# Kernel optimization log

Measured on AMD Instinct MI355X. Metric: run time of the kernel, lower is better.

The kernel has to match this reference:

```python
import jax, jax.numpy as jnp
import numpy as np

NEG_BIG = 10000000000.0  # matches tf source's -1e10 mask fill


def setup_inputs() -> dict:
    key = jax.random.key(0)
    k1, k2, k3 = jax.random.split(key, 3)
    B, H, T, D = 2, 12, 4096, 64
    return {
        "q": jax.random.normal(k1, (B, H, T, D), dtype=jnp.float32),
        "k": jax.random.normal(k2, (B, H, T, D), dtype=jnp.float32),
        "v": jax.random.normal(k3, (B, H, T, D), dtype=jnp.float32),
        "localAttention": 256,
    }


def _band_mask(nd, ns, local_attention, dtype):
    # 1's in the lower triangle counting from the lower-right corner,
    # optionally restricted to a local window of width `local_attention`.
    i = jnp.arange(nd)[:, None]
    j = jnp.arange(ns)[None, :]
    m = i >= j - ns + nd
    if local_attention > 0:
        m = m & (i < j - ns + nd + local_attention)
    return m.astype(dtype)


def reference(q, k, v, localAttention):
    # q,k,v: [B, H, T, D]
    dimv = v.shape[-1]
    w = jnp.einsum("bhqd,bhkd->bhqk", q, k) * (1.0 / np.sqrt(dimv))
    nd, ns = w.shape[2], w.shape[3]
    b = _band_mask(nd, ns, localAttention, w.dtype)[None, None]  # [1,1,nd,ns]
    w = w * b - jnp.asarray(NEG_BIG, w.dtype) * (1 - b)
    sm = jax.nn.softmax(w, axis=-1)
    out = jnp.einsum("bhqk,bhkd->bhqd", sm, v)       # [B,H,T,Dv]
    out = jnp.transpose(out, (0, 2, 1, 3))            # [B,T,H,Dv]
    B, T, H, Dv = out.shape
    return out.reshape(B, T, H * Dv)
```

## Files before the change

### kernel.cpp

```cpp
#include <hip/hip_runtime.h>

#define TT 4096
#define DD 64
#define HH 12
#define LAMAX 256
#define KT 64
#define VS 68

typedef __attribute__((ext_vector_type(8))) short s8v;
typedef __attribute__((ext_vector_type(4))) short s4v;
typedef __attribute__((ext_vector_type(2))) short s2v;
typedef __attribute__((ext_vector_type(4))) float f4v;

static __device__ __forceinline__ short f2bf(float f) {
  unsigned u = __builtin_bit_cast(unsigned, f);
  u += 0x7FFFu + ((u >> 16) & 1u);
  return (short)(u >> 16);
}

static __device__ __forceinline__ s8v pack8(float4 a, float4 b) {
  s8v r;
  r[0] = f2bf(a.x); r[1] = f2bf(a.y); r[2] = f2bf(a.z); r[3] = f2bf(a.w);
  r[4] = f2bf(b.x); r[5] = f2bf(b.y); r[6] = f2bf(b.z); r[7] = f2bf(b.w);
  return r;
}

static __device__ __forceinline__ s8v pack8s(float4 a, float4 b, float s) {
  s8v r;
  r[0] = f2bf(a.x * s); r[1] = f2bf(a.y * s); r[2] = f2bf(a.z * s); r[3] = f2bf(a.w * s);
  r[4] = f2bf(b.x * s); r[5] = f2bf(b.y * s); r[6] = f2bf(b.z * s); r[7] = f2bf(b.w * s);
  return r;
}

static __device__ __forceinline__ f4v MFMA16(s4v a, s4v b, f4v c) {
#if defined(__has_builtin) && __has_builtin(__builtin_amdgcn_mfma_f32_16x16x16bf16_1k)
  return __builtin_amdgcn_mfma_f32_16x16x16bf16_1k(a, b, c, 0, 0, 0);
#elif defined(__has_builtin) && __has_builtin(__builtin_amdgcn_mfma_f32_16x16x16_bf16)
  return __builtin_amdgcn_mfma_f32_16x16x16_bf16(a, b, c, 0, 0, 0);
#else
  asm("v_mfma_f32_16x16x16_bf16 %0, %1, %2, %0\n\ts_nop 7\n\ts_nop 7"
      : "+v"(c) : "v"(a), "v"(b));
  return c;
#endif
}

__global__ __launch_bounds__(256, 4)
void lma_attn_kernel(const float* __restrict__ Q, const float* __restrict__ K,
                     const float* __restrict__ V, const int* __restrict__ laPtr,
                     float* __restrict__ out)
{
  __shared__ short k_lds[2][64 * 64];
  __shared__ short vt_lds[2][64 * VS];

  const int tid  = threadIdx.x;
  const int lane = tid & 63;
  const int w    = tid >> 6;
  const int c    = lane & 15;
  const int g    = lane >> 4;

  const int bid = blockIdx.x;
  const int wg  = (bid & 7) * 192 + (bid >> 3);
  const int bh  = wg >> 6;
  const int q0  = (wg & 63) << 6;
  const int la  = laPtr[0];

  const size_t base = (size_t)bh * (TT * DD);
  const int rb    = q0 + w * 16;
  const int i_row = rb + c;

  const float SCL = 0.125f * 1.44269504f;
  s8v qf[2];
  {
    const float* qp = Q + base + (size_t)i_row * DD + 8 * g;
    qf[0] = pack8s(*(const float4*)qp,        *(const float4*)(qp + 4),  SCL);
    qf[1] = pack8s(*(const float4*)(qp + 32), *(const float4*)(qp + 36), SCL);
  }

  const int kj  = tid >> 2;
  const int kd0 = (tid & 3) << 4;
  const int vj0 = (tid & 31) << 1;
  const int vd0 = (tid >> 5) << 3;

  float4 kr0, kr1, kr2, kr3, vr0, vr1, vr2, vr3;
  auto stage_load = [&](int kj0) {
    const float* kp = K + base + (size_t)(kj0 + kj) * DD + kd0;
    kr0 = *(const float4*)kp;        kr1 = *(const float4*)(kp + 4);
    kr2 = *(const float4*)(kp + 8);  kr3 = *(const float4*)(kp + 12);
    const float* vp = V + base + (size_t)(kj0 + vj0) * DD + vd0;
    vr0 = *(const float4*)vp;        vr1 = *(const float4*)(vp + 4);
    vr2 = *(const float4*)(vp + DD); vr3 = *(const float4*)(vp + DD + 4);
  };
  auto stage_write = [&](int buf) {
    short* kb = (short*)k_lds[buf];
    const int sw = kj & 7, g8 = kd0 >> 3;
    *(s8v*)&kb[kj * 64 + ((g8    ) ^ sw) * 8] = pack8(kr0, kr1);
    *(s8v*)&kb[kj * 64 + ((g8 + 1) ^ sw) * 8] = pack8(kr2, kr3);
    short* vb = (short*)vt_lds[buf];
    const float a0[8] = {vr0.x, vr0.y, vr0.z, vr0.w, vr1.x, vr1.y, vr1.z, vr1.w};
    const float a1[8] = {vr2.x, vr2.y, vr2.z, vr2.w, vr3.x, vr3.y, vr3.z, vr3.w};
    #pragma unroll
    for (int e = 0; e < 8; ++e) {
      s2v pr; pr[0] = f2bf(a0[e]); pr[1] = f2bf(a1[e]);
      *(s2v*)&vb[(vd0 + e) * VS + vj0] = pr;
    }
  };

  f4v acc[4] = {};
  float m2   = -1e30f;
  float lsum = 0.f;

  const int t0 = (q0 >= LAMAX) ? 0 : ((LAMAX - q0) >> 6);

  stage_load(q0 - LAMAX + (t0 << 6));
  stage_write(t0 & 1);
  __syncthreads();

  for (int t = t0; t < 5; ++t) {
    const int kj0 = q0 - LAMAX + (t << 6);
    if (t < 4) stage_load(kj0 + KT);

    const short* kb = (const short*)k_lds[t & 1];
    const short* vb = (const short*)vt_lds[t & 1];

    if ((kj0 <= rb + 15) && (kj0 + KT >= rb - la + 2)) {
      f4v sa[4] = {};
      #pragma unroll
      for (int ch = 0; ch < 2; ++ch)
        #pragma unroll
        for (int ks = 0; ks < 4; ++ks) {
          s8v kf = *(const s8v*)&kb[(ks * 16 + c) * 64 + (((ch << 2) + g) ^ (c & 7)) * 8];
          sa[ks] = __builtin_amdgcn_mfma_f32_16x16x32_bf16(kf, qf[ch], sa[ks], 0, 0, 0);
        }

      const bool needC = (kj0 + 63 > rb);
      const bool needL = (kj0 < rb + 16 - la);
      const int jrel = kj0 - rb;
      const int jloR = i_row - la + 1;
      float p[4][4];
      #define MASKMAX(NC, NL)                                              \
        _Pragma("unroll")                                                  \
        for (int ks = 0; ks < 4; ++ks)                                     \
          _Pragma("unroll")                                                \
          for (int r = 0; r < 4; ++r) {                                    \
            float s = sa[ks][r];                                           \
            if (NC || NL) {                                                \
              const int jt = kj0 + ks * 16 + 4 * g + r;                    \
              bool ok = true;                                              \
              if (NC) ok = (jt <= i_row);                                  \
              if (NL) ok = ok && (jt >= jloR);                             \
              s = ok ? s : -1e30f;                                         \
            }                                                              \
            p[ks][r] = s;                                                  \
          }
      if (needC) { if (needL) { MASKMAX(true, true) } else { MASKMAX(true, false) } }
      else       { if (needL) { MASKMAX(false, true) } else { MASKMAX(false, false) } }
      #undef MASKMAX
      (void)jrel;

      float t0a = fmaxf(fmaxf(p[0][0], p[0][1]), fmaxf(p[0][2], p[0][3]));
      float t1a = fmaxf(fmaxf(p[1][0], p[1][1]), fmaxf(p[1][2], p[1][3]));
      float t2a = fmaxf(fmaxf(p[2][0], p[2][1]), fmaxf(p[2][2], p[2][3]));
      float t3a = fmaxf(fmaxf(p[3][0], p[3][1]), fmaxf(p[3][2], p[3][3]));
      float tmax = fmaxf(fmaxf(t0a, t1a), fmaxf(t2a, t3a));
      tmax = fmaxf(tmax, __shfl_xor(tmax, 16, 64));
      tmax = fmaxf(tmax, __shfl_xor(tmax, 32, 64));

      if (!__all(tmax <= m2 + 8.0f)) {
        const float mn = fmaxf(m2, tmax);
        const float corr = exp2f(m2 - mn);
        m2 = mn;
        lsum *= corr;
        #pragma unroll
        for (int dt = 0; dt < 4; ++dt) {
          acc[dt][0] *= corr; acc[dt][1] *= corr;
          acc[dt][2] *= corr; acc[dt][3] *= corr;
        }
      }

      s4v pb[4]; float e[4][4];
      #pragma unroll
      for (int ks = 0; ks < 4; ++ks)
        #pragma unroll
        for (int r = 0; r < 4; ++r) {
          e[ks][r] = exp2f(p[ks][r] - m2);
          pb[ks][r] = f2bf(e[ks][r]);
        }

      #pragma unroll
      for (int dt = 0; dt < 4; ++dt) {
        const int d = dt * 16 + c;
        #pragma unroll
        for (int sub = 0; sub < 4; ++sub) {
          s4v vf = *(const s4v*)&vb[d * VS + sub * 16 + g * 4];
          acc[dt] = MFMA16(vf, pb[sub], acc[dt]);
        }
      }

      float s0 = (e[0][0] + e[0][1]) + (e[0][2] + e[0][3]);
      float s1 = (e[1][0] + e[1][1]) + (e[1][2] + e[1][3]);
      float s2 = (e[2][0] + e[2][1]) + (e[2][2] + e[2][3]);
      float s3 = (e[3][0] + e[3][1]) + (e[3][2] + e[3][3]);
      float ps = (s0 + s1) + (s2 + s3);
      ps += __shfl_xor(ps, 16, 64);
      ps += __shfl_xor(ps, 32, 64);
      lsum += ps;
    }

    if (t < 4) stage_write((t + 1) & 1);
    __syncthreads();
  }

  const float inv = 1.f / lsum;
  float* op = out + ((size_t)(bh / HH) * TT + i_row) * (HH * DD) + (bh % HH) * DD + 4 * g;
  #pragma unroll
  for (int dt = 0; dt < 4; ++dt) {
    float4 o;
    o.x = acc[dt][0] * inv; o.y = acc[dt][1] * inv;
    o.z = acc[dt][2] * inv; o.w = acc[dt][3] * inv;
    *(float4*)(op + dt * 16) = o;
  }
}

extern "C" void kernel_launch(void* const* d_in, const int* in_sizes, int n_in,
                              void* d_out, int out_size, void* d_ws, size_t ws_size,
                              hipStream_t stream) {
  const float* q = (const float*)d_in[0];
  const float* k = (const float*)d_in[1];
  const float* v = (const float*)d_in[2];
  const int* la = (const int*)d_in[3];
  float* out = (float*)d_out;
  (void)in_sizes; (void)n_in; (void)out_size; (void)d_ws; (void)ws_size;

  dim3 grid(24 * 64);
  dim3 block(256);
  lma_attn_kernel<<<grid, block, 0, stream>>>(q, k, v, la, out);
}
```

Measured before the change: 143.2 us.

## Halve key tile to 32 rows, use packed bf16 conversion and raise occupancy

Shrinks the K/V tile from 64 to 32 keys and runs 10 iterations instead of 5, so blocks skip more of the band that lies outside the mask and use less LDS and fewer registers. Launch bounds rise to 6 waves per SIMD. Scalar bf16 rounding is replaced with packed float2-to-bf16 conversion and the hardware exp2 builtin. The XCD-aware block remap is removed. In exchange there are more barriers and more, smaller loads per output row.

```diff
diff --git a/kernel.cpp b/kernel.cpp
--- a/kernel.cpp
+++ b/kernel.cpp
@@ -1,42 +1,43 @@
 #include <hip/hip_runtime.h>
+#include <hip/hip_bf16.h>
 
 #define TT 4096
 #define DD 64
 #define HH 12
 #define LAMAX 256
-#define KT 64
-#define VS 68
+#define KT 32
+#define NT 10
+#define VS 36
 
 typedef __attribute__((ext_vector_type(8))) short s8v;
 typedef __attribute__((ext_vector_type(4))) short s4v;
 typedef __attribute__((ext_vector_type(2))) short s2v;
 typedef __attribute__((ext_vector_type(4))) float f4v;
 
-static __device__ __forceinline__ short f2bf(float f) {
-  unsigned u = __builtin_bit_cast(unsigned, f);
-  u += 0x7FFFu + ((u >> 16) & 1u);
-  return (short)(u >> 16);
+static __device__ __forceinline__ unsigned pk2(float a, float b) {
+  __hip_bfloat162 h = __float22bfloat162_rn(make_float2(a, b));
+  unsigned u;
+  __builtin_memcpy(&u, &h, sizeof(u));
+  return u;
 }
 
 static __device__ __forceinline__ s8v pack8(float4 a, float4 b) {
-  s8v r;
-  r[0] = f2bf(a.x); r[1] = f2bf(a.y); r[2] = f2bf(a.z); r[3] = f2bf(a.w);
-  r[4] = f2bf(b.x); r[5] = f2bf(b.y); r[6] = f2bf(b.z); r[7] = f2bf(b.w);
-  return r;
+  union { unsigned u[4]; s8v s; } r;
+  r.u[0] = pk2(a.x, a.y); r.u[1] = pk2(a.z, a.w);
+  r.u[2] = pk2(b.x, b.y); r.u[3] = pk2(b.z, b.w);
+  return r.s;
 }
 
 static __device__ __forceinline__ s8v pack8s(float4 a, float4 b, float s) {
-  s8v r;
-  r[0] = f2bf(a.x * s); r[1] = f2bf(a.y * s); r[2] = f2bf(a.z * s); r[3] = f2bf(a.w * s);
-  r[4] = f2bf(b.x * s); r[5] = f2bf(b.y * s); r[6] = f2bf(b.z * s); r[7] = f2bf(b.w * s);
-  return r;
+  union { unsigned u[4]; s8v r; } o;
+  o.u[0] = pk2(a.x * s, a.y * s); o.u[1] = pk2(a.z * s, a.w * s);
+  o.u[2] = pk2(b.x * s, b.y * s); o.u[3] = pk2(b.z * s, b.w * s);
+  return o.r;
 }
 
 static __device__ __forceinline__ f4v MFMA16(s4v a, s4v b, f4v c) {
 #if defined(__has_builtin) && __has_builtin(__builtin_amdgcn_mfma_f32_16x16x16bf16_1k)
   return __builtin_amdgcn_mfma_f32_16x16x16bf16_1k(a, b, c, 0, 0, 0);
-#elif defined(__has_builtin) && __has_builtin(__builtin_amdgcn_mfma_f32_16x16x16_bf16)
-  return __builtin_amdgcn_mfma_f32_16x16x16_bf16(a, b, c, 0, 0, 0);
 #else
   asm("v_mfma_f32_16x16x16_bf16 %0, %1, %2, %0\n\ts_nop 7\n\ts_nop 7"
       : "+v"(c) : "v"(a), "v"(b));
@@ -44,12 +45,12 @@
 #endif
 }
 
-__global__ __launch_bounds__(256, 4)
+__global__ __launch_bounds__(256, 6)
 void lma_attn_kernel(const float* __restrict__ Q, const float* __restrict__ K,
                      const float* __restrict__ V, const int* __restrict__ laPtr,
                      float* __restrict__ out)
 {
-  __shared__ short k_lds[2][64 * 64];
+  __shared__ short k_lds[2][KT * 64];
   __shared__ short vt_lds[2][64 * VS];
 
   const int tid  = threadIdx.x;
@@ -59,9 +60,8 @@
   const int g    = lane >> 4;
 
   const int bid = blockIdx.x;
-  const int wg  = (bid & 7) * 192 + (bid >> 3);
-  const int bh  = wg >> 6;
-  const int q0  = (wg & 63) << 6;
+  const int bh  = bid >> 6;
+  const int q0  = (bid & 63) << 6;
   const int la  = laPtr[0];
 
   const size_t base = (size_t)bh * (TT * DD);
@@ -76,32 +76,28 @@
     qf[1] = pack8s(*(const float4*)(qp + 32), *(const float4*)(qp + 36), SCL);
   }
 
-  const int kj  = tid >> 2;
-  const int kd0 = (tid & 3) << 4;
-  const int vj0 = (tid & 31) << 1;
-  const int vd0 = (tid >> 5) << 3;
-
-  float4 kr0, kr1, kr2, kr3, vr0, vr1, vr2, vr3;
+  const int kj  = tid >> 3;
+  const int kd0 = (tid & 7) << 3;
+  const int vj0 = (tid & 15) << 1;
+  const int vd0 = (tid >> 4) << 2;
+
+  float4 kr0, kr1, vr0, vr1;
   auto stage_load = [&](int kj0) {
     const float* kp = K + base + (size_t)(kj0 + kj) * DD + kd0;
-    kr0 = *(const float4*)kp;        kr1 = *(const float4*)(kp + 4);
-    kr2 = *(const float4*)(kp + 8);  kr3 = *(const float4*)(kp + 12);
+    kr0 = *(const float4*)kp; kr1 = *(const float4*)(kp + 4);
     const float* vp = V + base + (size_t)(kj0 + vj0) * DD + vd0;
-    vr0 = *(const float4*)vp;        vr1 = *(const float4*)(vp + 4);
-    vr2 = *(const float4*)(vp + DD); vr3 = *(const float4*)(vp + DD + 4);
+    vr0 = *(const float4*)vp; vr1 = *(const float4*)(vp + DD);
   };
   auto stage_write = [&](int buf) {
-    short* kb = (short*)k_lds[buf];
-    const int sw = kj & 7, g8 = kd0 >> 3;
-    *(s8v*)&kb[kj * 64 + ((g8    ) ^ sw) * 8] = pack8(kr0, kr1);
-    *(s8v*)&kb[kj * 64 + ((g8 + 1) ^ sw) * 8] = pack8(kr2, kr3);
-    short* vb = (short*)vt_lds[buf];
-    const float a0[8] = {vr0.x, vr0.y, vr0.z, vr0.w, vr1.x, vr1.y, vr1.z, vr1.w};
-    const float a1[8] = {vr2.x, vr2.y, vr2.z, vr2.w, vr3.x, vr3.y, vr3.z, vr3.w};
+    *(s8v*)&k_lds[buf][kj * 64 + (((tid & 7) ^ (kj & 7)) << 3)] = pack8(kr0, kr1);
+    const float a0[4] = {vr0.x, vr0.y, vr0.z, vr0.w};
+    const float a1[4] = {vr1.x, vr1.y, vr1.z, vr1.w};
     #pragma unroll
-    for (int e = 0; e < 8; ++e) {
-      s2v pr; pr[0] = f2bf(a0[e]); pr[1] = f2bf(a1[e]);
-      *(s2v*)&vb[(vd0 + e) * VS + vj0] = pr;
+    for (int e = 0; e < 4; ++e) {
+      unsigned pr = pk2(a0[e], a1[e]);
+      s2v prv;
+      __builtin_memcpy(&prv, &pr, sizeof(prv));
+      *(s2v*)&vt_lds[buf][(vd0 + e) * VS + vj0] = prv;
     }
   };
 
@@ -109,37 +105,36 @@
   float m2   = -1e30f;
   float lsum = 0.f;
 
-  const int t0 = (q0 >= LAMAX) ? 0 : ((LAMAX - q0) >> 6);
-
-  stage_load(q0 - LAMAX + (t0 << 6));
+  const int t0 = (q0 >= LAMAX) ? 0 : ((LAMAX - q0) >> 5);
+
+  stage_load(q0 - LAMAX + (t0 << 5));
   stage_write(t0 & 1);
   __syncthreads();
 
-  for (int t = t0; t < 5; ++t) {
-    const int kj0 = q0 - LAMAX + (t << 6);
-    if (t < 4) stage_load(kj0 + KT);
-
-    const short* kb = (const short*)k_lds[t & 1];
-    const short* vb = (const short*)vt_lds[t & 1];
+  for (int t = t0; t < NT; ++t) {
+    const int kj0 = q0 - LAMAX + (t << 5);
+    if (t + 1 < NT) stage_load(kj0 + KT);
+
+    const short* kb = k_lds[t & 1];
+    const short* vb = vt_lds[t & 1];
 
     if ((kj0 <= rb + 15) && (kj0 + KT >= rb - la + 2)) {
-      f4v sa[4] = {};
+      f4v sa[2] = {};
       #pragma unroll
       for (int ch = 0; ch < 2; ++ch)
         #pragma unroll
-        for (int ks = 0; ks < 4; ++ks) {
-          s8v kf = *(const s8v*)&kb[(ks * 16 + c) * 64 + (((ch << 2) + g) ^ (c & 7)) * 8];
+        for (int ks = 0; ks < 2; ++ks) {
+          s8v kf = *(const s8v*)&kb[(ks * 16 + c) * 64 + ((((ch << 2) + g) ^ (c & 7)) << 3)];
           sa[ks] = __builtin_amdgcn_mfma_f32_16x16x32_bf16(kf, qf[ch], sa[ks], 0, 0, 0);
         }
 
-      const bool needC = (kj0 + 63 > rb);
+      const bool needC = (kj0 + KT - 1 > rb);
       const bool needL = (kj0 < rb + 16 - la);
-      const int jrel = kj0 - rb;
       const int jloR = i_row - la + 1;
-      float p[4][4];
-      #define MASKMAX(NC, NL)                                              \
+      float p[2][4];
+      #define MASKP(NC, NL)                                                \
         _Pragma("unroll")                                                  \
-        for (int ks = 0; ks < 4; ++ks)                                     \
+        for (int ks = 0; ks < 2; ++ks)                                     \
           _Pragma("unroll")                                                \
           for (int r = 0; r < 4; ++r) {                                    \
             float s = sa[ks][r];                                           \
@@ -152,22 +147,18 @@
             }                                                              \
             p[ks][r] = s;                                                  \
           }
-      if (needC) { if (needL) { MASKMAX(true, true) } else { MASKMAX(true, false) } }
-      else       { if (needL) { MASKMAX(false, true) } else { MASKMAX(false, false) } }
-      #undef MASKMAX
-      (void)jrel;
-
-      float t0a = fmaxf(fmaxf(p[0][0], p[0][1]), fmaxf(p[0][2], p[0][3]));
-      float t1a = fmaxf(fmaxf(p[1][0], p[1][1]), fmaxf(p[1][2], p[1][3]));
-      float t2a = fmaxf(fmaxf(p[2][0], p[2][1]), fmaxf(p[2][2], p[2][3]));
-      float t3a = fmaxf(fmaxf(p[3][0], p[3][1]), fmaxf(p[3][2], p[3][3]));
-      float tmax = fmaxf(fmaxf(t0a, t1a), fmaxf(t2a, t3a));
+      if (needC) { if (needL) { MASKP(true, true) } else { MASKP(true, false) } }
+      else       { if (needL) { MASKP(false, true) } else { MASKP(false, false) } }
+      #undef MASKP
+
+      float tmax = fmaxf(fmaxf(fmaxf(p[0][0], p[0][1]), fmaxf(p[0][2], p[0][3])),
+                         fmaxf(fmaxf(p[1][0], p[1][1]), fmaxf(p[1][2], p[1][3])));
       tmax = fmaxf(tmax, __shfl_xor(tmax, 16, 64));
       tmax = fmaxf(tmax, __shfl_xor(tmax, 32, 64));
 
       if (!__all(tmax <= m2 + 8.0f)) {
         const float mn = fmaxf(m2, tmax);
-        const float corr = exp2f(m2 - mn);
+        const float corr = __builtin_amdgcn_exp2f(m2 - mn);
         m2 = mn;
         lsum *= corr;
         #pragma unroll
@@ -177,36 +168,39 @@
         }
       }
 
-      s4v pb[4]; float e[4][4];
-      #pragma unroll
-      for (int ks = 0; ks < 4; ++ks)
-        #pragma unroll
-        for (int r = 0; r < 4; ++r) {
-          e[ks][r] = exp2f(p[ks][r] - m2);
-          pb[ks][r] = f2bf(e[ks][r]);
-        }
+      float e[2][4];
+      #pragma unroll
+      for (int ks = 0; ks < 2; ++ks)
+        #pragma unroll
+        for (int r = 0; r < 4; ++r)
+          e[ks][r] = __builtin_amdgcn_exp2f(p[ks][r] - m2);
+      s4v pb[2];
+      #pragma unroll
+      for (int ks = 0; ks < 2; ++ks) {
+        union { unsigned u[2]; s4v s; } pp;
+        pp.u[0] = pk2(e[ks][0], e[ks][1]);
+        pp.u[1] = pk2(e[ks][2], e[ks][3]);
+        pb[ks] = pp.s;
+      }
 
       #pragma unroll
       for (int dt = 0; dt < 4; ++dt) {
         const int d = dt * 16 + c;
         #pragma unroll
-        for (int sub = 0; sub < 4; ++sub) {
-          s4v vf = *(const s4v*)&vb[d * VS + sub * 16 + g * 4];
+        for (int sub = 0; sub < 2; ++sub) {
+          s4v vf = *(const s4v*)&vb[d * VS + sub * 16 + 4 * g];
           acc[dt] = MFMA16(vf, pb[sub], acc[dt]);
         }
       }
 
-      float s0 = (e[0][0] + e[0][1]) + (e[0][2] + e[0][3]);
-      float s1 = (e[1][0] + e[1][1]) + (e[1][2] + e[1][3]);
-      float s2 = (e[2][0] + e[2][1]) + (e[2][2] + e[2][3]);
-      float s3 = (e[3][0] + e[3][1]) + (e[3][2] + e[3][3]);
-      float ps = (s0 + s1) + (s2 + s3);
+      float ps = ((e[0][0] + e[0][1]) + (e[0][2] + e[0][3])) +
+                 ((e[1][0] + e[1][1]) + (e[1][2] + e[1][3]));
       ps += __shfl_xor(ps, 16, 64);
       ps += __shfl_xor(ps, 32, 64);
       lsum += ps;
     }
 
-    if (t < 4) stage_write((t + 1) & 1);
+    if (t + 1 < NT) stage_write((t + 1) & 1);
     __syncthreads();
   }
 
```

Measured after the change: 164.2 us. +14.7%, slower.
